# Optimization experiments

Hardware: AMD Instinct MI355X
Metric: run time of the kernel (lower is better)

Reference implementation:

```python
import jax, jax.numpy as jnp
import numpy as np

D = 128  # chunk_embSize

def _mlp_one_layer(x, W, b):
    # MLP_one_layer in eval mode: dropout is identity -> tanh(x @ W^T + b)
    return jnp.tanh(x @ W.T + b)

def setup_inputs() -> dict:
    key = jax.random.key(0)
    ks = jax.random.split(key, 10)
    n_item, n_opi, n_user, L = 50000, 5000, 10000, 50
    s = 0.02  # initializer_range-style scale for linear weights
    return {
        "item_table": jax.random.normal(ks[0], (n_item, D), jnp.float32),
        "opin_table": jax.random.normal(ks[1], (n_opi, D), jnp.float32),
        "user_emb": jax.random.normal(ks[2], (n_user, D), jnp.float32),
        "attr_embedding": jax.random.normal(ks[3], (D,), jnp.float32),
        "Wq": jax.random.normal(ks[4], (D, D), jnp.float32) * s,
        "bq": jnp.zeros((D,), jnp.float32),
        "Wk": jax.random.normal(ks[5], (D, D), jnp.float32) * s,
        "bk": jnp.zeros((D,), jnp.float32),
        "Wv": jax.random.normal(ks[6], (D, D), jnp.float32) * s,
        "bv": jnp.zeros((D,), jnp.float32),
        "item_seqs": jax.random.randint(ks[7], (n_user, L), 0, n_item, jnp.int64),
        "opin_seqs": jax.random.randint(ks[8], (n_user, L), 0, n_opi, jnp.int64),
    }

def reference(item_table, opin_table, user_emb, attr_embedding,
              Wq, bq, Wk, bk, Wv, bv, item_seqs, opin_seqs):
    # FineRec UiMatrix.opin_update_ui (eval mode: all dropouts identity)
    item_emb = item_table[item_seqs]          # [U, L, D] gather
    opin_emb = opin_table[opin_seqs]          # [U, L, D] gather
    # k = k_layer(attr + item); v = v_layer(item + opin); q = q_layer(user)
    k_emb = _mlp_one_layer(attr_embedding[None, None, :] + item_emb, Wk, bk)
    v_emb = _mlp_one_layer(item_emb + opin_emb, Wv, bv)
    q_emb = _mlp_one_layer(user_emb, Wq, bq)  # [U, D]
    # unnormalized attention weights over the user's interaction sequence
    w_agg = jnp.einsum("ud,uld->ul", q_emb, k_emb)  # [U, L]
    mask = (item_seqs > 0).astype(w_agg.dtype)       # padding mask
    w_agg = w_agg * mask
    # weighted aggregation over sequence -> new user embedding
    user_embedding = jnp.einsum("ul,uld->ud", w_agg, v_emb)  # [U, D]
    return user_embedding
```

## Files before the change

kernel.cpp:

```cpp
#include <hip/hip_runtime.h>
#include <hip/hip_bf16.h>
#include <stdint.h>

typedef __attribute__((ext_vector_type(8))) short bf16x8;
typedef __attribute__((ext_vector_type(4))) float f32x4;

#define S_2LOG2E 2.8853900817779268f

#if __has_builtin(__builtin_amdgcn_exp2f)
#define EXP2F(x) __builtin_amdgcn_exp2f(x)
#else
#define EXP2F(x) __expf((x) * 0.6931471805599453f)
#endif
#if __has_builtin(__builtin_amdgcn_rcpf)
#define RCPF(x) __builtin_amdgcn_rcpf(x)
#else
#define RCPF(x) (1.0f / (x))
#endif

__device__ __forceinline__ float tanh_fast(float x) {
    float e = __expf(2.0f * x);
    return 1.0f - 2.0f / (e + 1.0f);
}

__device__ __forceinline__ bf16x8 pack2(float4 a, float4 b) {
    union { bf16x8 v; __hip_bfloat162 h[4]; } r;
    r.h[0] = __float22bfloat162_rn(make_float2(a.x, a.y));
    r.h[1] = __float22bfloat162_rn(make_float2(a.z, a.w));
    r.h[2] = __float22bfloat162_rn(make_float2(b.x, b.y));
    r.h[3] = __float22bfloat162_rn(make_float2(b.z, b.w));
    return r.v;
}
__device__ __forceinline__ float4 scl4(float4 a) {
    a.x *= S_2LOG2E; a.y *= S_2LOG2E; a.z *= S_2LOG2E; a.w *= S_2LOG2E;
    return a;
}
#define MFMA16(a, b, c) __builtin_amdgcn_mfma_f32_16x16x32_bf16((a), (b), (c), 0, 0, 0)

__global__ void finerec_prep(
    const float* __restrict__ user_emb, const float* __restrict__ attr,
    const float* __restrict__ Wq, const float* __restrict__ bq,
    const float* __restrict__ Wk, const float* __restrict__ bk,
    const float* __restrict__ Wv, const float* __restrict__ bv,
    const float* __restrict__ item_table, const float* __restrict__ opin_table,
    float* __restrict__ q_ws, float* __restrict__ bkz_ws, float* __restrict__ bvz_ws,
    short* __restrict__ wf_ws, short* __restrict__ itb, short* __restrict__ opb,
    float* __restrict__ out, int U, int n_item, int n_opi, int qb)
{
    const int bx = blockIdx.x, tid = threadIdx.x;
    if (bx >= qb + 49) {
        const int castb = gridDim.x - qb - 49;
        const int gid = (bx - qb - 49) * 256 + tid;
        const int stride = castb * 256;
        const int tci = n_item * 16, tc = (n_item + n_opi) * 16;
        for (int c = gid; c < tc; c += stride) {
            if (c < tci) {
                const float* src = item_table + (size_t)c * 8;
                ((bf16x8*)itb)[c] = pack2(*(const float4*)src, *(const float4*)(src + 4));
            } else {
                const float* src = opin_table + (size_t)(c - tci) * 8;
                ((bf16x8*)opb)[c - tci] = pack2(*(const float4*)src, *(const float4*)(src + 4));
            }
        }
        return;
    }
    if (bx >= qb + 9) {
        const int gid = (bx - qb - 9) * 256 + tid;
        float4 z = {0.0f, 0.0f, 0.0f, 0.0f};
        for (int i = gid; i < U * 32; i += 40 * 256) ((float4*)out)[i] = z;
        return;
    }
    if (bx >= qb + 1) {
        const int bi = bx - qb - 1;
#pragma unroll
        for (int t = 0; t < 2; ++t) {
            const int g = bi * 512 + t * 256 + tid;
            const int mat = g >> 11, gg = g & 2047, r = gg >> 4, c = gg & 15;
            const float* src = (mat ? Wv : Wk) + r * 128 + c * 8;
            ((bf16x8*)wf_ws)[(mat << 11) + (r << 4) + (c ^ (r & 15))] =
                pack2(scl4(*(const float4*)src), scl4(*(const float4*)(src + 4)));
        }
        return;
    }
    if (bx == qb) {
        if (tid < 128) {
            const float* wr = Wk + tid * 128;
            float s = bk[tid];
            for (int k = 0; k < 128; k += 4) {
                float4 w4 = *(const float4*)(wr + k);
                float4 a4 = *(const float4*)(attr + k);
                s += w4.x * a4.x + w4.y * a4.y + w4.z * a4.z + w4.w * a4.w;
            }
            bkz_ws[tid] = s * S_2LOG2E;
        } else if (tid < 256) {
            bvz_ws[tid - 128] = bv[tid - 128] * S_2LOG2E;
        }
        return;
    }
    const int wv = tid >> 6, lane = tid & 63;
    const int l15 = lane & 15, quad = lane >> 4;
    const int u0 = (bx * 4 + wv) * 16;
    int ur = u0 + l15; if (ur >= U) ur = U - 1;
    const float* up = user_emb + (size_t)ur * 128 + quad * 8;
    bf16x8 af[4];
#pragma unroll
    for (int ks = 0; ks < 4; ++ks)
        af[ks] = pack2(*(const float4*)(up + ks * 32), *(const float4*)(up + ks * 32 + 4));
#pragma unroll
    for (int nt = 0; nt < 8; ++nt) {
        const int n = nt * 16 + l15;
        const float* wp = Wq + n * 128 + quad * 8;
        f32x4 acc = {0, 0, 0, 0};
#pragma unroll
        for (int ks = 0; ks < 4; ++ks) {
            bf16x8 bf = pack2(*(const float4*)(wp + ks * 32), *(const float4*)(wp + ks * 32 + 4));
            acc = MFMA16(af[ks], bf, acc);
        }
        const float bqv = bq[n];
#pragma unroll
        for (int r = 0; r < 4; ++r) {
            int row = u0 + quad * 4 + r;
            if (row < U) q_ws[row * 128 + nt * 16 + l15] = tanh_fast(acc[r] + bqv);
        }
    }
}

template<int BF16, int LC>
__global__ __launch_bounds__(1024, 4) void finerec_main(
    const float* __restrict__ item_table, const float* __restrict__ opin_table,
    const int* __restrict__ item_seqs, const int* __restrict__ opin_seqs,
    const float* __restrict__ q_ws, const float* __restrict__ bkz_ws,
    const float* __restrict__ bvz_ws, const short* __restrict__ wf_ws,
    const short* __restrict__ itb, const short* __restrict__ opb,
    float* __restrict__ out, int U, int Lrt)
{
    __shared__ __align__(16) short wlds[32768];
    __shared__ float bkz_lds[128], bvz_lds[128];

    const int L = LC ? LC : Lrt;
    const int tid = threadIdx.x;
    const int wv = tid >> 6, lane = tid & 63, l15 = lane & 15, quad = lane >> 4;

    const bf16x8* wsrc = (const bf16x8*)wf_ws;
    bf16x8* wldsv = (bf16x8*)wlds;
#pragma unroll
    for (int i = 0; i < 4; ++i)
        wldsv[i * 1024 + tid] = wsrc[i * 1024 + tid];
    if (tid < 128)      bkz_lds[tid]       = bkz_ws[tid];
    else if (tid < 256) bvz_lds[tid - 128] = bvz_ws[tid - 128];
    __syncthreads();

    const int UL = U * L;
    const int njobs = (UL + 15) >> 4;
    const int nwaves = gridDim.x * 16;

#pragma unroll 1
    for (int job = blockIdx.x * 16 + wv; job < njobs; job += nwaves) {
        const int js = __builtin_amdgcn_readfirstlane(job);
        const int g0 = js << 4;
        const int uA = g0 / L;
        const int bb = L - (g0 - uA * L);
        const bool split = (bb < 16) && (uA + 1 < U);

        int vi = 0, vo = 0;
        if (lane < 16 && g0 + lane < UL) {
            vi = item_seqs[g0 + lane];
            vo = opin_seqs[g0 + lane];
        }
        const unsigned long long mb = __ballot(vi > 0);

        const int idx = __shfl(vi, l15);
        bf16x8 ai[4];
        if (BF16) {
            const bf16x8* pb = (const bf16x8*)itb + (size_t)idx * 16 + quad;
#pragma unroll
            for (int ks = 0; ks < 4; ++ks) ai[ks] = pb[ks * 4];
        } else {
            const float* p = item_table + (size_t)idx * 128 + quad * 8;
#pragma unroll
            for (int ks = 0; ks < 4; ++ks)
                ai[ks] = pack2(*(const float4*)(p + ks * 32), *(const float4*)(p + ks * 32 + 4));
        }

        const float* qpA = q_ws + (size_t)uA * 128;

        float wacc[4] = {0.0f, 0.0f, 0.0f, 0.0f};
        if (!split) {
            float sq = 0.0f;
#pragma unroll 1
            for (int nt = 0; nt < 8; ++nt) {
                const int n = nt * 16 + l15;
                const float qa = qpA[n];
                const float bz = bkz_lds[n];
                f32x4 c = {bz, bz, bz, bz};
#pragma unroll
                for (int ks = 0; ks < 4; ++ks)
                    c = MFMA16(ai[ks], wldsv[(n << 4) + ((ks * 4 + quad) ^ l15)], c);
                const float m2qa = -2.0f * qa;
                sq += qa;
#pragma unroll
                for (int r = 0; r < 4; ++r) {
                    const float rc = RCPF(EXP2F(c[r]) + 1.0f);
                    wacc[r] = fmaf(m2qa, rc, wacc[r]);
                }
            }
#pragma unroll
            for (int r = 0; r < 4; ++r) wacc[r] += sq;
        } else {
            float sqA = 0.0f, sqB = 0.0f;
#pragma unroll 1
            for (int nt = 0; nt < 8; ++nt) {
                const int n = nt * 16 + l15;
                const float qa  = qpA[n];
                const float qb2 = qpA[128 + n];
                const float bz = bkz_lds[n];
                f32x4 c = {bz, bz, bz, bz};
#pragma unroll
                for (int ks = 0; ks < 4; ++ks)
                    c = MFMA16(ai[ks], wldsv[(n << 4) + ((ks * 4 + quad) ^ l15)], c);
                const float m2qa = -2.0f * qa, m2qb = -2.0f * qb2;
                sqA += qa; sqB += qb2;
#pragma unroll
                for (int r = 0; r < 4; ++r) {
                    const float rc = RCPF(EXP2F(c[r]) + 1.0f);
                    wacc[r] = fmaf((quad * 4 + r < bb) ? m2qa : m2qb, rc, wacc[r]);
                }
            }
#pragma unroll
            for (int r = 0; r < 4; ++r) wacc[r] += (quad * 4 + r < bb) ? sqA : sqB;
        }
        float w[4];
#pragma unroll
        for (int r = 0; r < 4; ++r) {
            float t = wacc[r];
            t += __shfl_xor(t, 1); t += __shfl_xor(t, 2);
            t += __shfl_xor(t, 4); t += __shfl_xor(t, 8);
            w[r] = ((mb >> (quad * 4 + r)) & 1ull) ? t : 0.0f;
        }
        const int od = __shfl(vo, l15);
        bf16x8 ao[4];
        if (BF16) {
            const bf16x8* pb = (const bf16x8*)opb + (size_t)od * 16 + quad;
#pragma unroll
            for (int ks = 0; ks < 4; ++ks) ao[ks] = pb[ks * 4];
        } else {
            const float* p = opin_table + (size_t)od * 128 + quad * 8;
#pragma unroll
            for (int ks = 0; ks < 4; ++ks)
                ao[ks] = pack2(*(const float4*)(p + ks * 32), *(const float4*)(p + ks * 32 + 4));
        }
        float m2w[4]; float wsum = 0.0f;
#pragma unroll
        for (int r = 0; r < 4; ++r) { m2w[r] = -2.0f * w[r]; wsum += w[r]; }
        float* outbase = out + (size_t)uA * 128 + quad * 32 + l15;
        if (!split) {
            float s0 = 0.0f, s1 = 0.0f;
#pragma unroll 1
            for (int nt = 0; nt < 8; ++nt) {
                const int n = nt * 16 + l15;
                const float bz = bvz_lds[n];
                f32x4 c = {bz, bz, bz, bz};
#pragma unroll
                for (int ks = 0; ks < 4; ++ks) {
                    const bf16x8 wf = wldsv[2048 + (n << 4) + ((ks * 4 + quad) ^ l15)];
                    c = MFMA16(ai[ks], wf, c);
                    c = MFMA16(ao[ks], wf, c);
                }
                float acc = wsum;
#pragma unroll
                for (int r = 0; r < 4; ++r) {
                    const float rc = RCPF(EXP2F(c[r]) + 1.0f);
                    acc = fmaf(m2w[r], rc, acc);
                }
                acc += __shfl_xor(acc, 16);
                acc += __shfl_xor(acc, 32);
                const bool mine = (quad == (nt >> 1));
                s0 += (mine && !(nt & 1)) ? acc : 0.0f;
                s1 += (mine &&  (nt & 1)) ? acc : 0.0f;
            }
            atomicAdd(outbase, s0);
            atomicAdd(outbase + 16, s1);
        } else {
            float m2wA[4]; float wsA = 0.0f;
#pragma unroll
            for (int r = 0; r < 4; ++r) {
                const bool sA = (quad * 4 + r) < bb;
                m2wA[r] = sA ? m2w[r] : 0.0f;
                wsA += sA ? w[r] : 0.0f;
            }
            float sA0 = 0.0f, sA1 = 0.0f, sB0 = 0.0f, sB1 = 0.0f;
#pragma unroll 1
            for (int nt = 0; nt < 8; ++nt) {
                const int n = nt * 16 + l15;
                const float bz = bvz_lds[n];
                f32x4 c = {bz, bz, bz, bz};
#pragma unroll
                for (int ks = 0; ks < 4; ++ks) {
                    const bf16x8 wf = wldsv[2048 + (n << 4) + ((ks * 4 + quad) ^ l15)];
                    c = MFMA16(ai[ks], wf, c);
                    c = MFMA16(ao[ks], wf, c);
                }
                float accT = wsum, accA = wsA;
#pragma unroll
                for (int r = 0; r < 4; ++r) {
                    const float rc = RCPF(EXP2F(c[r]) + 1.0f);
                    accT = fmaf(m2w[r],  rc, accT);
                    accA = fmaf(m2wA[r], rc, accA);
                }
                accT += __shfl_xor(accT, 16); accT += __shfl_xor(accT, 32);
                accA += __shfl_xor(accA, 16); accA += __shfl_xor(accA, 32);
                const float accB = accT - accA;
                const bool mine = (quad == (nt >> 1));
                const bool lo = !(nt & 1);
                sA0 += (mine && lo)  ? accA : 0.0f;
                sA1 += (mine && !lo) ? accA : 0.0f;
                sB0 += (mine && lo)  ? accB : 0.0f;
                sB1 += (mine && !lo) ? accB : 0.0f;
            }
            atomicAdd(outbase, sA0);
            atomicAdd(outbase + 16, sA1);
            atomicAdd(outbase + 128, sB0);
            atomicAdd(outbase + 144, sB1);
        }
    }
}

extern "C" void kernel_launch(void* const* d_in, const int* in_sizes, int n_in,
                              void* d_out, int out_size, void* d_ws, size_t ws_size,
                              hipStream_t stream) {
    const float* item_table = (const float*)d_in[0];
    const float* opin_table = (const float*)d_in[1];
    const float* user_emb   = (const float*)d_in[2];
    const float* attr       = (const float*)d_in[3];
    const float* Wq = (const float*)d_in[4];
    const float* bq = (const float*)d_in[5];
    const float* Wk = (const float*)d_in[6];
    const float* bk = (const float*)d_in[7];
    const float* Wv = (const float*)d_in[8];
    const float* bv = (const float*)d_in[9];
    const int* item_seqs = (const int*)d_in[10];
    const int* opin_seqs = (const int*)d_in[11];
    float* out = (float*)d_out;

    const int U = in_sizes[2] / 128;
    const int L = in_sizes[10] / U;
    const int n_item = in_sizes[0] / 128;
    const int n_opi  = in_sizes[1] / 128;

    char* w = (char*)d_ws;
    float* q_ws   = (float*)w;               w += (size_t)U * 128 * 4;
    float* bkz_ws = (float*)w;               w += 512;
    float* bvz_ws = (float*)w;               w += 512;
    short* wf_ws  = (short*)w;               w += 4096 * 16;
    short* itb    = (short*)w;               w += (size_t)n_item * 128 * 2;
    short* opb    = (short*)w;               w += (size_t)n_opi * 128 * 2;
    const size_t need = (size_t)(w - (char*)d_ws);
    const int use_bf16 = (ws_size >= need) ? 1 : 0;

    const int qb = (U + 63) / 64;
    const int castb = use_bf16 ? (((n_item + n_opi) * 16 + 255) / 256) : 0;
    const int prep_grid = qb + 49 + castb;
    finerec_prep<<<prep_grid, 256, 0, stream>>>(
        user_emb, attr, Wq, bq, Wk, bk, Wv, bv, item_table, opin_table,
        q_ws, bkz_ws, bvz_ws, wf_ws, itb, opb, out, U, n_item, n_opi, qb);

    if (use_bf16) {
        if (L == 50)
            finerec_main<1, 50><<<512, 1024, 0, stream>>>(
                item_table, opin_table, item_seqs, opin_seqs,
                q_ws, bkz_ws, bvz_ws, wf_ws, itb, opb, out, U, L);
        else
            finerec_main<1, 0><<<512, 1024, 0, stream>>>(
                item_table, opin_table, item_seqs, opin_seqs,
                q_ws, bkz_ws, bvz_ws, wf_ws, itb, opb, out, U, L);
    } else {
        if (L == 50)
            finerec_main<0, 50><<<512, 1024, 0, stream>>>(
                item_table, opin_table, item_seqs, opin_seqs,
                q_ws, bkz_ws, bvz_ws, wf_ws, itb, opb, out, U, L);
        else
            finerec_main<0, 0><<<512, 1024, 0, stream>>>(
                item_table, opin_table, item_seqs, opin_seqs,
                q_ws, bkz_ws, bvz_ws, wf_ws, itb, opb, out, U, L);
    }
}
```

Before: 183.1 us.

## Process two 16-row tiles per wave to reuse LDS weight fragments

```diff
diff --git a/kernel.cpp b/kernel.cpp
--- a/kernel.cpp
+++ b/kernel.cpp
@@ -126,7 +126,7 @@
 }
 
 template<int BF16, int LC>
-__global__ __launch_bounds__(1024, 4) void finerec_main(
+__global__ __launch_bounds__(512, 4) void finerec_main(
     const float* __restrict__ item_table, const float* __restrict__ opin_table,
     const int* __restrict__ item_seqs, const int* __restrict__ opin_seqs,
     const float* __restrict__ q_ws, const float* __restrict__ bkz_ws,
@@ -144,47 +144,51 @@
     const bf16x8* wsrc = (const bf16x8*)wf_ws;
     bf16x8* wldsv = (bf16x8*)wlds;
 #pragma unroll
-    for (int i = 0; i < 4; ++i)
-        wldsv[i * 1024 + tid] = wsrc[i * 1024 + tid];
+    for (int i = 0; i < 8; ++i)
+        wldsv[i * 512 + tid] = wsrc[i * 512 + tid];
     if (tid < 128)      bkz_lds[tid]       = bkz_ws[tid];
     else if (tid < 256) bvz_lds[tid - 128] = bvz_ws[tid - 128];
     __syncthreads();
 
     const int UL = U * L;
-    const int njobs = (UL + 15) >> 4;
-    const int nwaves = gridDim.x * 16;
+    const int njobs = (UL + 31) >> 5;
+    const int nwaves = gridDim.x * 8;
 
 #pragma unroll 1
-    for (int job = blockIdx.x * 16 + wv; job < njobs; job += nwaves) {
-        const int js = __builtin_amdgcn_readfirstlane(job);
-        const int g0 = js << 4;
+    for (int job = blockIdx.x * 8 + wv; job < njobs; job += nwaves) {
+        const int g0 = job << 5;
         const int uA = g0 / L;
         const int bb = L - (g0 - uA * L);
-        const bool split = (bb < 16) && (uA + 1 < U);
+        const bool split = (bb < 32) && (uA + 1 < U);
 
         int vi = 0, vo = 0;
-        if (lane < 16 && g0 + lane < UL) {
+        if (lane < 32 && g0 + lane < UL) {
             vi = item_seqs[g0 + lane];
             vo = opin_seqs[g0 + lane];
         }
         const unsigned long long mb = __ballot(vi > 0);
 
-        const int idx = __shfl(vi, l15);
-        bf16x8 ai[4];
+        const int idxL = __shfl(vi, l15);
+        const int idxH = __shfl(vi, l15 + 16);
+        bf16x8 aiL[4], aiH[4];
         if (BF16) {
-            const bf16x8* pb = (const bf16x8*)itb + (size_t)idx * 16 + quad;
-#pragma unroll
-            for (int ks = 0; ks < 4; ++ks) ai[ks] = pb[ks * 4];
+            const bf16x8* pL = (const bf16x8*)itb + (size_t)idxL * 16 + quad;
+            const bf16x8* pH = (const bf16x8*)itb + (size_t)idxH * 16 + quad;
+#pragma unroll
+            for (int ks = 0; ks < 4; ++ks) { aiL[ks] = pL[ks * 4]; aiH[ks] = pH[ks * 4]; }
         } else {
-            const float* p = item_table + (size_t)idx * 128 + quad * 8;
-#pragma unroll
-            for (int ks = 0; ks < 4; ++ks)
-                ai[ks] = pack2(*(const float4*)(p + ks * 32), *(const float4*)(p + ks * 32 + 4));
+            const float* pL = item_table + (size_t)idxL * 128 + quad * 8;
+            const float* pH = item_table + (size_t)idxH * 128 + quad * 8;
+#pragma unroll
+            for (int ks = 0; ks < 4; ++ks) {
+                aiL[ks] = pack2(*(const float4*)(pL + ks * 32), *(const float4*)(pL + ks * 32 + 4));
+                aiH[ks] = pack2(*(const float4*)(pH + ks * 32), *(const float4*)(pH + ks * 32 + 4));
+            }
         }
 
         const float* qpA = q_ws + (size_t)uA * 128;
 
-        float wacc[4] = {0.0f, 0.0f, 0.0f, 0.0f};
+        float waccL[4] = {0, 0, 0, 0}, waccH[4] = {0, 0, 0, 0};
         if (!split) {
             float sq = 0.0f;
 #pragma unroll 1
@@ -192,20 +196,25 @@
                 const int n = nt * 16 + l15;
                 const float qa = qpA[n];
                 const float bz = bkz_lds[n];
-                f32x4 c = {bz, bz, bz, bz};
-#pragma unroll
-                for (int ks = 0; ks < 4; ++ks)
-                    c = MFMA16(ai[ks], wldsv[(n << 4) + ((ks * 4 + quad) ^ l15)], c);
+                f32x4 cL = {bz, bz, bz, bz}, cH = {bz, bz, bz, bz};
+#pragma unroll
+                for (int ks = 0; ks < 4; ++ks) {
+                    const bf16x8 wf = wldsv[(n << 4) + ((ks * 4 + quad) ^ l15)];
+                    cL = MFMA16(aiL[ks], wf, cL);
+                    cH = MFMA16(aiH[ks], wf, cH);
+                }
                 const float m2qa = -2.0f * qa;
                 sq += qa;
 #pragma unroll
                 for (int r = 0; r < 4; ++r) {
-                    const float rc = RCPF(EXP2F(c[r]) + 1.0f);
-                    wacc[r] = fmaf(m2qa, rc, wacc[r]);
-                }
-            }
-#pragma unroll
-            for (int r = 0; r < 4; ++r) wacc[r] += sq;
+                    const float rcL = RCPF(EXP2F(cL[r]) + 1.0f);
+                    const float rcH = RCPF(EXP2F(cH[r]) + 1.0f);
+                    waccL[r] = fmaf(m2qa, rcL, waccL[r]);
+                    waccH[r] = fmaf(m2qa, rcH, waccH[r]);
+                }
+            }
+#pragma unroll
+            for (int r = 0; r < 4; ++r) { waccL[r] += sq; waccH[r] += sq; }
         } else {
             float sqA = 0.0f, sqB = 0.0f;
 #pragma unroll 1
@@ -214,44 +223,64 @@
                 const float qa  = qpA[n];
                 const float qb2 = qpA[128 + n];
                 const float bz = bkz_lds[n];
-                f32x4 c = {bz, bz, bz, bz};
-#pragma unroll
-                for (int ks = 0; ks < 4; ++ks)
-                    c = MFMA16(ai[ks], wldsv[(n << 4) + ((ks * 4 + quad) ^ l15)], c);
+                f32x4 cL = {bz, bz, bz, bz}, cH = {bz, bz, bz, bz};
+#pragma unroll
+                for (int ks = 0; ks < 4; ++ks) {
+                    const bf16x8 wf = wldsv[(n << 4) + ((ks * 4 + quad) ^ l15)];
+                    cL = MFMA16(aiL[ks], wf, cL);
+                    cH = MFMA16(aiH[ks], wf, cH);
+                }
                 const float m2qa = -2.0f * qa, m2qb = -2.0f * qb2;
                 sqA += qa; sqB += qb2;
 #pragma unroll
                 for (int r = 0; r < 4; ++r) {
-                    const float rc = RCPF(EXP2F(c[r]) + 1.0f);
-                    wacc[r] = fmaf((quad * 4 + r < bb) ? m2qa : m2qb, rc, wacc[r]);
-                }
-            }
-#pragma unroll
-            for (int r = 0; r < 4; ++r) wacc[r] += (quad * 4 + r < bb) ? sqA : sqB;
-        }
-        float w[4];
+                    const float rcL = RCPF(EXP2F(cL[r]) + 1.0f);
+                    const float rcH = RCPF(EXP2F(cH[r]) + 1.0f);
+                    waccL[r] = fmaf((quad * 4 + r      < bb) ? m2qa : m2qb, rcL, waccL[r]);
+                    waccH[r] = fmaf((quad * 4 + r + 16 < bb) ? m2qa : m2qb, rcH, waccH[r]);
+                }
+            }
+#pragma unroll
+            for (int r = 0; r < 4; ++r) {
+                waccL[r] += (quad * 4 + r      < bb) ? sqA : sqB;
+                waccH[r] += (quad * 4 + r + 16 < bb) ? sqA : sqB;
+            }
+        }
+        float wL[4], wH[4];
 #pragma unroll
         for (int r = 0; r < 4; ++r) {
-            float t = wacc[r];
+            float t = waccL[r];
             t += __shfl_xor(t, 1); t += __shfl_xor(t, 2);
             t += __shfl_xor(t, 4); t += __shfl_xor(t, 8);
-            w[r] = ((mb >> (quad * 4 + r)) & 1ull) ? t : 0.0f;
-        }
-        const int od = __shfl(vo, l15);
-        bf16x8 ao[4];
+            wL[r] = ((mb >> (quad * 4 + r)) & 1ull) ? t : 0.0f;
+            float u = waccH[r];
+            u += __shfl_xor(u, 1); u += __shfl_xor(u, 2);
+            u += __shfl_xor(u, 4); u += __shfl_xor(u, 8);
+            wH[r] = ((mb >> (16 + quad * 4 + r)) & 1ull) ? u : 0.0f;
+        }
+        const int odL = __shfl(vo, l15);
+        const int odH = __shfl(vo, l15 + 16);
+        bf16x8 aoL[4], aoH[4];
         if (BF16) {
-            const bf16x8* pb = (const bf16x8*)opb + (size_t)od * 16 + quad;
-#pragma unroll
-            for (int ks = 0; ks < 4; ++ks) ao[ks] = pb[ks * 4];
+            const bf16x8* pL = (const bf16x8*)opb + (size_t)odL * 16 + quad;
+            const bf16x8* pH = (const bf16x8*)opb + (size_t)odH * 16 + quad;
+#pragma unroll
+            for (int ks = 0; ks < 4; ++ks) { aoL[ks] = pL[ks * 4]; aoH[ks] = pH[ks * 4]; }
         } else {
-            const float* p = opin_table + (size_t)od * 128 + quad * 8;
-#pragma unroll
-            for (int ks = 0; ks < 4; ++ks)
-                ao[ks] = pack2(*(const float4*)(p + ks * 32), *(const float4*)(p + ks * 32 + 4));
-        }
-        float m2w[4]; float wsum = 0.0f;
-#pragma unroll
-        for (int r = 0; r < 4; ++r) { m2w[r] = -2.0f * w[r]; wsum += w[r]; }
+            const float* pL = opin_table + (size_t)odL * 128 + quad * 8;
+            const float* pH = opin_table + (size_t)odH * 128 + quad * 8;
+#pragma unroll
+            for (int ks = 0; ks < 4; ++ks) {
+                aoL[ks] = pack2(*(const float4*)(pL + ks * 32), *(const float4*)(pL + ks * 32 + 4));
+                aoH[ks] = pack2(*(const float4*)(pH + ks * 32), *(const float4*)(pH + ks * 32 + 4));
+            }
+        }
+        float m2wL[4], m2wH[4]; float wsL = 0.0f, wsH = 0.0f;
+#pragma unroll
+        for (int r = 0; r < 4; ++r) {
+            m2wL[r] = -2.0f * wL[r]; wsL += wL[r];
+            m2wH[r] = -2.0f * wH[r]; wsH += wH[r];
+        }
         float* outbase = out + (size_t)uA * 128 + quad * 32 + l15;
         if (!split) {
             float s0 = 0.0f, s1 = 0.0f;
@@ -259,19 +288,24 @@
             for (int nt = 0; nt < 8; ++nt) {
                 const int n = nt * 16 + l15;
                 const float bz = bvz_lds[n];
-                f32x4 c = {bz, bz, bz, bz};
+                f32x4 cL = {bz, bz, bz, bz}, cH = {bz, bz, bz, bz};
 #pragma unroll
                 for (int ks = 0; ks < 4; ++ks) {
                     const bf16x8 wf = wldsv[2048 + (n << 4) + ((ks * 4 + quad) ^ l15)];
-                    c = MFMA16(ai[ks], wf, c);
-                    c = MFMA16(ao[ks], wf, c);
-                }
-                float acc = wsum;
+                    cL = MFMA16(aiL[ks], wf, cL);
+                    cL = MFMA16(aoL[ks], wf, cL);
+                    cH = MFMA16(aiH[ks], wf, cH);
+                    cH = MFMA16(aoH[ks], wf, cH);
+                }
+                float accL = wsL, accH = wsH;
 #pragma unroll
                 for (int r = 0; r < 4; ++r) {
-                    const float rc = RCPF(EXP2F(c[r]) + 1.0f);
-                    acc = fmaf(m2w[r], rc, acc);
-                }
+                    const float rcL = RCPF(EXP2F(cL[r]) + 1.0f);
+                    const float rcH = RCPF(EXP2F(cH[r]) + 1.0f);
+                    accL = fmaf(m2wL[r], rcL, accL);
+                    accH = fmaf(m2wH[r], rcH, accH);
+                }
+                float acc = accL + accH;
                 acc += __shfl_xor(acc, 16);
                 acc += __shfl_xor(acc, 32);
                 const bool mine = (quad == (nt >> 1));
@@ -281,32 +315,40 @@
             atomicAdd(outbase, s0);
             atomicAdd(outbase + 16, s1);
         } else {
-            float m2wA[4]; float wsA = 0.0f;
+            float m2wAL[4], m2wAH[4]; float wsAL = 0.0f, wsAH = 0.0f;
 #pragma unroll
             for (int r = 0; r < 4; ++r) {
-                const bool sA = (quad * 4 + r) < bb;
-                m2wA[r] = sA ? m2w[r] : 0.0f;
-                wsA += sA ? w[r] : 0.0f;
+                const bool sL = (quad * 4 + r)      < bb;
+                const bool sH = (quad * 4 + r + 16) < bb;
+                m2wAL[r] = sL ? m2wL[r] : 0.0f; wsAL += sL ? wL[r] : 0.0f;
+                m2wAH[r] = sH ? m2wH[r] : 0.0f; wsAH += sH ? wH[r] : 0.0f;
             }
             float sA0 = 0.0f, sA1 = 0.0f, sB0 = 0.0f, sB1 = 0.0f;
 #pragma unroll 1
             for (int nt = 0; nt < 8; ++nt) {
                 const int n = nt * 16 + l15;
                 const float bz = bvz_lds[n];
-                f32x4 c = {bz, bz, bz, bz};
+                f32x4 cL = {bz, bz, bz, bz}, cH = {bz, bz, bz, bz};
 #pragma unroll
                 for (int ks = 0; ks < 4; ++ks) {
                     const bf16x8 wf = wldsv[2048 + (n << 4) + ((ks * 4 + quad) ^ l15)];
-                    c = MFMA16(ai[ks], wf, c);
-                    c = MFMA16(ao[ks], wf, c);
-                }
-                float accT = wsum, accA = wsA;
+                    cL = MFMA16(aiL[ks], wf, cL);
+                    cL = MFMA16(aoL[ks], wf, cL);
+                    cH = MFMA16(aiH[ks], wf, cH);
+                    cH = MFMA16(aoH[ks], wf, cH);
+                }
+                float accTL = wsL, accTH = wsH, accAL = wsAL, accAH = wsAH;
 #pragma unroll
                 for (int r = 0; r < 4; ++r) {
-                    const float rc = RCPF(EXP2F(c[r]) + 1.0f);
-                    accT = fmaf(m2w[r],  rc, accT);
-                    accA = fmaf(m2wA[r], rc, accA);
-                }
+                    const float rcL = RCPF(EXP2F(cL[r]) + 1.0f);
+                    const float rcH = RCPF(EXP2F(cH[r]) + 1.0f);
+                    accTL = fmaf(m2wL[r],  rcL, accTL);
+                    accAL = fmaf(m2wAL[r], rcL, accAL);
+                    accTH = fmaf(m2wH[r],  rcH, accTH);
+                    accAH = fmaf(m2wAH[r], rcH, accAH);
+                }
+                float accT = accTL + accTH;
+                float accA = accAL + accAH;
                 accT += __shfl_xor(accT, 16); accT += __shfl_xor(accT, 32);
                 accA += __shfl_xor(accA, 16); accA += __shfl_xor(accA, 32);
                 const float accB = accT - accA;
@@ -366,20 +408,20 @@
 
     if (use_bf16) {
         if (L == 50)
-            finerec_main<1, 50><<<512, 1024, 0, stream>>>(
+            finerec_main<1, 50><<<512, 512, 0, stream>>>(
                 item_table, opin_table, item_seqs, opin_seqs,
                 q_ws, bkz_ws, bvz_ws, wf_ws, itb, opb, out, U, L);
         else
-            finerec_main<1, 0><<<512, 1024, 0, stream>>>(
+            finerec_main<1, 0><<<512, 512, 0, stream>>>(
                 item_table, opin_table, item_seqs, opin_seqs,
                 q_ws, bkz_ws, bvz_ws, wf_ws, itb, opb, out, U, L);
     } else {
         if (L == 50)
-            finerec_main<0, 50><<<512, 1024, 0, stream>>>(
+            finerec_main<0, 50><<<512, 512, 0, stream>>>(
                 item_table, opin_table, item_seqs, opin_seqs,
                 q_ws, bkz_ws, bvz_ws, wf_ws, itb, opb, out, U, L);
         else
-            finerec_main<0, 0><<<512, 1024, 0, stream>>>(
+            finerec_main<0, 0><<<512, 512, 0, stream>>>(
                 item_table, opin_table, item_seqs, opin_seqs,
                 q_ws, bkz_ws, bvz_ws, wf_ws, itb, opb, out, U, L);
     }
```

New measurement: 206.2 us. +12.7%, slower.
